# Kernel tuning notes

Hardware: AMD Instinct MI355X
Metric: run time of the kernel (lower is better)

The kernel has to match this reference:

```python
import jax, jax.numpy as jnp
import numpy as np

N_QUERY, N_BACKGND, DIM = 2048, 8192, 32


def setup_inputs() -> dict:
    key = jax.random.key(0)
    k0, k1, k2, k3 = jax.random.split(key, 4)
    x_backgnd = jax.random.normal(k0, (N_BACKGND, DIM), dtype=jnp.float32)
    y_backgnd = jax.random.normal(k1, (N_BACKGND,), dtype=jnp.float32)
    x_query = jax.random.normal(k2, (N_QUERY, DIM), dtype=jnp.float32)
    r = jax.random.uniform(k3, (N_QUERY, N_BACKGND), dtype=jnp.float32)
    sigma = jnp.array([0.1], dtype=jnp.float32)      # nn.Parameter init_sigma
    r_scale = jnp.array([3.0], dtype=jnp.float32)    # nn.Parameter init_r_scale
    w = jnp.ones((DIM,), dtype=jnp.float32)          # trainable weights matrix
    return {"x_backgnd": x_backgnd, "y_backgnd": y_backgnd, "x_query": x_query,
            "r": r, "sigma": sigma, "r_scale": r_scale, "w": w}


def reference(x_backgnd, y_backgnd, x_query, r, sigma, r_scale, w):
    # weighted Euclidean distance: ||(xq - xb) * w|| via the expansion trick,
    # avoiding the (n_query, n_backgnd, dim) difference tensor.
    xq = x_query * w           # (nq, d)
    xb = x_backgnd * w         # (nb, d)
    q2 = jnp.sum(xq * xq, axis=1, keepdims=True)        # (nq, 1)
    b2 = jnp.sum(xb * xb, axis=1)                        # (nb,)
    d2 = q2 + b2[None, :] - 2.0 * (xq @ xb.T)            # (nq, nb)
    dists = jnp.sqrt(jnp.maximum(d2, 0.0))
    # exp kernel with relationship bias, normalize, weighted sum
    k_vals = jnp.exp(-dists / sigma + r_scale * r)       # sigma, r_scale broadcast (1,)
    k_sum = jnp.sum(k_vals, axis=1, keepdims=True) + 1e-8
    weights = k_vals / k_sum
    y_pred = weights @ y_backgnd                          # (nq,)
    return y_pred
```

## Files before the change

kernel.cpp:

```cpp
#include <hip/hip_runtime.h>
#include <math.h>

#define NQ 2048
#define NB 8192
#define DIM 32

#define LOG2E 1.44269504088896340736f

typedef _Float16 half8 __attribute__((ext_vector_type(8)));
typedef float    f32x4 __attribute__((ext_vector_type(4)));

#define WS_ACC 0
#define WS_Q2  16384
#define WS_B2  24576
#define WS_XQH 57344
#define WS_XBH 188416

__global__ __launch_bounds__(256) void relnw_pre(
    const float* __restrict__ xq, const float* __restrict__ xb,
    const float* __restrict__ w,
    _Float16* __restrict__ XQh, _Float16* __restrict__ XBh,
    float* __restrict__ q2, float* __restrict__ b2)
{
    int i = blockIdx.x * 256 + threadIdx.x;
    const float* src; _Float16* dst; float* s2;
    if (i < NQ)            { src = xq + (size_t)i * DIM;        dst = XQh + (size_t)i * DIM;        s2 = q2 + i; }
    else if (i < NQ + NB)  { int j = i - NQ;
                             src = xb + (size_t)j * DIM;        dst = XBh + (size_t)j * DIM;        s2 = b2 + j; }
    else return;
    float s = 0.f;
#pragma unroll
    for (int d = 0; d < DIM; ++d) {
        float t = src[d] * w[d];
        _Float16 h = (_Float16)t;
        float th = (float)h;
        s = fmaf(th, th, s);
        dst[d] = h;
    }
    *s2 = s;
}

#define BT_PER_WAVE 16
#define BG_PER_WAVE (BT_PER_WAVE * 16)

__global__ __launch_bounds__(256) void relnw_main(
    const _Float16* __restrict__ XQh,
    const _Float16* __restrict__ XBh,
    const float* __restrict__ q2,
    const float* __restrict__ b2,
    const float* __restrict__ yb,
    const float* __restrict__ r,
    const float* __restrict__ sigma,
    const float* __restrict__ rscale,
    float* __restrict__ acc)
{
    const int tid  = threadIdx.x;
    const int lane = tid & 63;
    const int wid  = tid >> 6;
    const int m    = lane & 15;
    const int quad = lane >> 4;

    const int q0     = blockIdx.y * 16;
    const int bstart = (blockIdx.x * 4 + wid) * BG_PER_WAVE;

    const float c1 = -LOG2E / sigma[0];
    const float c2 =  LOG2E * rscale[0];

    const half8 afrag = *(const half8*)(XQh + (size_t)(q0 + m) * DIM + quad * 8);

    float q2r[4];
#pragma unroll
    for (int g = 0; g < 4; ++g) q2r[g] = q2[q0 + quad * 4 + g];

    const _Float16* xbp = XBh + (size_t)(bstart + m) * DIM + quad * 8;
    const float*    rp  = r + (size_t)(q0 + quad * 4) * NB + bstart + m;

    float sk[4]  = {0.f, 0.f, 0.f, 0.f};
    float sky[4] = {0.f, 0.f, 0.f, 0.f};

#pragma unroll
    for (int it = 0; it < BT_PER_WAVE; ++it) {
        const int bc = bstart + it * 16 + m;
        const half8 bfrag = *(const half8*)(xbp + (size_t)it * 16 * DIM);
        const float yv  = yb[bc];
        const float b2v = b2[bc];
        float rr[4];
#pragma unroll
        for (int g = 0; g < 4; ++g) rr[g] = rp[(size_t)g * NB + it * 16];

        f32x4 dot = __builtin_amdgcn_mfma_f32_16x16x32_f16(
            afrag, bfrag, (f32x4){0.f, 0.f, 0.f, 0.f}, 0, 0, 0);

#pragma unroll
        for (int g = 0; g < 4; ++g) {
            float d2 = fmaf(-2.f, dot[g], q2r[g] + b2v);
            d2 = fmaxf(d2, 0.f);
            float dist = __builtin_amdgcn_sqrtf(d2);
            float e = fmaf(dist, c1, rr[g] * c2);
            float k = __builtin_amdgcn_exp2f(e);
            sk[g] += k;
            sky[g] = fmaf(k, yv, sky[g]);
        }
    }

#pragma unroll
    for (int off = 1; off <= 8; off <<= 1) {
#pragma unroll
        for (int g = 0; g < 4; ++g) {
            sk[g]  += __shfl_xor(sk[g],  off, 64);
            sky[g] += __shfl_xor(sky[g], off, 64);
        }
    }
    if (m == 0) {
#pragma unroll
        for (int g = 0; g < 4; ++g) {
            atomicAdd(acc + (q0 + quad * 4 + g),      sk[g]);
            atomicAdd(acc + NQ + (q0 + quad * 4 + g), sky[g]);
        }
    }
}

__global__ __launch_bounds__(256) void relnw_finalize(
    const float* __restrict__ acc, float* __restrict__ out)
{
    int q = blockIdx.x * 256 + threadIdx.x;
    if (q < NQ)
        out[q] = acc[NQ + q] / (acc[q] + 1e-8f);
}

extern "C" void kernel_launch(void* const* d_in, const int* in_sizes, int n_in,
                              void* d_out, int out_size, void* d_ws, size_t ws_size,
                              hipStream_t stream) {
    const float* xb     = (const float*)d_in[0];
    const float* yb     = (const float*)d_in[1];
    const float* xq     = (const float*)d_in[2];
    const float* r      = (const float*)d_in[3];
    const float* sigma  = (const float*)d_in[4];
    const float* rscale = (const float*)d_in[5];
    const float* w      = (const float*)d_in[6];
    float* out = (float*)d_out;

    char* ws = (char*)d_ws;
    float*    acc = (float*)(ws + WS_ACC);
    float*    q2  = (float*)(ws + WS_Q2);
    float*    b2  = (float*)(ws + WS_B2);
    _Float16* XQh = (_Float16*)(ws + WS_XQH);
    _Float16* XBh = (_Float16*)(ws + WS_XBH);

    hipMemsetAsync(acc, 0, 2 * NQ * sizeof(float), stream);

    relnw_pre<<<(NQ + NB + 255) / 256, 256, 0, stream>>>(xq, xb, w, XQh, XBh, q2, b2);

    dim3 grid(NB / (4 * BG_PER_WAVE), NQ / 16);
    relnw_main<<<grid, 256, 0, stream>>>(XQh, XBh, q2, b2, yb, r, sigma, rscale, acc);

    relnw_finalize<<<(NQ + 255) / 256, 256, 0, stream>>>(acc, out);
}
```

Measured before the change: 117.0 us.

## Tile two query blocks per wave and fold accumulator zeroing into prep kernel

Each wave now computes two 16-query tiles against the same background fragment, so each loaded XB fragment, y and b2 value is reused across twice as many queries. The background span per wave is halved so the grid stays the same size. Separately, the accumulator memset is replaced by zeroing inside the preprocessing kernel, which drops one stream operation. Register pressure rises because accumulators and r loads are doubled, and the dominant r traffic is unchanged.

Measured after the change: 119.9 us. 2.4% more time.

```diff
diff --git a/kernel.cpp b/kernel.cpp
--- a/kernel.cpp
+++ b/kernel.cpp
@@ -20,13 +20,15 @@
     const float* __restrict__ xq, const float* __restrict__ xb,
     const float* __restrict__ w,
     _Float16* __restrict__ XQh, _Float16* __restrict__ XBh,
-    float* __restrict__ q2, float* __restrict__ b2)
+    float* __restrict__ q2, float* __restrict__ b2,
+    float* __restrict__ acc)
 {
     int i = blockIdx.x * 256 + threadIdx.x;
+    if (i < 2 * NQ) acc[i] = 0.f;
     const float* src; _Float16* dst; float* s2;
-    if (i < NQ)            { src = xq + (size_t)i * DIM;        dst = XQh + (size_t)i * DIM;        s2 = q2 + i; }
+    if (i < NQ)            { src = xq + (size_t)i * DIM;  dst = XQh + (size_t)i * DIM;  s2 = q2 + i; }
     else if (i < NQ + NB)  { int j = i - NQ;
-                             src = xb + (size_t)j * DIM;        dst = XBh + (size_t)j * DIM;        s2 = b2 + j; }
+                             src = xb + (size_t)j * DIM;  dst = XBh + (size_t)j * DIM;  s2 = b2 + j; }
     else return;
     float s = 0.f;
 #pragma unroll
@@ -40,8 +42,9 @@
     *s2 = s;
 }
 
-#define BT_PER_WAVE 16
+#define BT_PER_WAVE 8
 #define BG_PER_WAVE (BT_PER_WAVE * 16)
+#define QT 2
 
 __global__ __launch_bounds__(256) void relnw_main(
     const _Float16* __restrict__ XQh,
@@ -60,23 +63,26 @@
     const int m    = lane & 15;
     const int quad = lane >> 4;
 
-    const int q0     = blockIdx.y * 16;
+    const int q0     = blockIdx.y * (16 * QT);
     const int bstart = (blockIdx.x * 4 + wid) * BG_PER_WAVE;
 
     const float c1 = -LOG2E / sigma[0];
     const float c2 =  LOG2E * rscale[0];
 
-    const half8 afrag = *(const half8*)(XQh + (size_t)(q0 + m) * DIM + quad * 8);
-
-    float q2r[4];
+    half8 afrag[QT];
+    float q2r[QT][4];
 #pragma unroll
-    for (int g = 0; g < 4; ++g) q2r[g] = q2[q0 + quad * 4 + g];
+    for (int t = 0; t < QT; ++t) {
+        afrag[t] = *(const half8*)(XQh + (size_t)(q0 + t * 16 + m) * DIM + quad * 8);
+#pragma unroll
+        for (int g = 0; g < 4; ++g) q2r[t][g] = q2[q0 + t * 16 + quad * 4 + g];
+    }
 
     const _Float16* xbp = XBh + (size_t)(bstart + m) * DIM + quad * 8;
     const float*    rp  = r + (size_t)(q0 + quad * 4) * NB + bstart + m;
 
-    float sk[4]  = {0.f, 0.f, 0.f, 0.f};
-    float sky[4] = {0.f, 0.f, 0.f, 0.f};
+    float sk[QT][4]  = {};
+    float sky[QT][4] = {};
 
 #pragma unroll
     for (int it = 0; it < BT_PER_WAVE; ++it) {
@@ -84,39 +90,49 @@
         const half8 bfrag = *(const half8*)(xbp + (size_t)it * 16 * DIM);
         const float yv  = yb[bc];
         const float b2v = b2[bc];
-        float rr[4];
+        float rr[QT][4];
 #pragma unroll
-        for (int g = 0; g < 4; ++g) rr[g] = rp[(size_t)g * NB + it * 16];
-
-        f32x4 dot = __builtin_amdgcn_mfma_f32_16x16x32_f16(
-            afrag, bfrag, (f32x4){0.f, 0.f, 0.f, 0.f}, 0, 0, 0);
+        for (int t = 0; t < QT; ++t)
+#pragma unroll
+            for (int g = 0; g < 4; ++g)
+                rr[t][g] = rp[(size_t)(t * 16 + g) * NB + it * 16];
 
 #pragma unroll
-        for (int g = 0; g < 4; ++g) {
-            float d2 = fmaf(-2.f, dot[g], q2r[g] + b2v);
-            d2 = fmaxf(d2, 0.f);
-            float dist = __builtin_amdgcn_sqrtf(d2);
-            float e = fmaf(dist, c1, rr[g] * c2);
-            float k = __builtin_amdgcn_exp2f(e);
-            sk[g] += k;
-            sky[g] = fmaf(k, yv, sky[g]);
+        for (int t = 0; t < QT; ++t) {
+            f32x4 dot = __builtin_amdgcn_mfma_f32_16x16x32_f16(
+                afrag[t], bfrag, (f32x4){0.f, 0.f, 0.f, 0.f}, 0, 0, 0);
+#pragma unroll
+            for (int g = 0; g < 4; ++g) {
+                float d2 = fmaf(-2.f, dot[g], q2r[t][g] + b2v);
+                d2 = fmaxf(d2, 0.f);
+                float dist = __builtin_amdgcn_sqrtf(d2);
+                float e = fmaf(dist, c1, rr[t][g] * c2);
+                float k = __builtin_amdgcn_exp2f(e);
+                sk[t][g] += k;
+                sky[t][g] = fmaf(k, yv, sky[t][g]);
+            }
         }
     }
 
 #pragma unroll
     for (int off = 1; off <= 8; off <<= 1) {
 #pragma unroll
-        for (int g = 0; g < 4; ++g) {
-            sk[g]  += __shfl_xor(sk[g],  off, 64);
-            sky[g] += __shfl_xor(sky[g], off, 64);
-        }
+        for (int t = 0; t < QT; ++t)
+#pragma unroll
+            for (int g = 0; g < 4; ++g) {
+                sk[t][g]  += __shfl_xor(sk[t][g],  off, 64);
+                sky[t][g] += __shfl_xor(sky[t][g], off, 64);
+            }
     }
     if (m == 0) {
 #pragma unroll
-        for (int g = 0; g < 4; ++g) {
-            atomicAdd(acc + (q0 + quad * 4 + g),      sk[g]);
-            atomicAdd(acc + NQ + (q0 + quad * 4 + g), sky[g]);
-        }
+        for (int t = 0; t < QT; ++t)
+#pragma unroll
+            for (int g = 0; g < 4; ++g) {
+                int q = q0 + t * 16 + quad * 4 + g;
+                atomicAdd(acc + q,      sk[t][g]);
+                atomicAdd(acc + NQ + q, sky[t][g]);
+            }
     }
 }
 
@@ -147,11 +163,9 @@
     _Float16* XQh = (_Float16*)(ws + WS_XQH);
     _Float16* XBh = (_Float16*)(ws + WS_XBH);
 
-    hipMemsetAsync(acc, 0, 2 * NQ * sizeof(float), stream);
+    relnw_pre<<<(NQ + NB + 255) / 256, 256, 0, stream>>>(xq, xb, w, XQh, XBh, q2, b2, acc);
 
-    relnw_pre<<<(NQ + NB + 255) / 256, 256, 0, stream>>>(xq, xb, w, XQh, XBh, q2, b2);
-
-    dim3 grid(NB / (4 * BG_PER_WAVE), NQ / 16);
+    dim3 grid(NB / (4 * BG_PER_WAVE), NQ / (16 * QT));
     relnw_main<<<grid, 256, 0, stream>>>(XQh, XBh, q2, b2, yb, r, sigma, rscale, acc);
 
     relnw_finalize<<<(NQ + 255) / 256, 256, 0, stream>>>(acc, out);
```

## Fuse memset and finalize into pre/main kernels, fold distance terms into MFMA

Applied to the files above, without the earlier changes.

The accumulator zeroing moves into the preprocessing kernel, and the finalize kernel is replaced by a last-block-done counter inside the main kernel. This removes the memset and one kernel launch. The preprocessing kernel now uses four threads per row with vectorized float4 loads, half8 stores and a shuffle reduction. The background vectors are pre-scaled by -2 so the MFMA accumulator starts at q2+b2 and directly yields d2, saving per-element FMAs. The changes add an atomic counter, a threadfence and a serialized tail on the last block. Folding -2 into fp16 is exact.

Result: slower. 144.6 us (+23.5%).

```diff
diff --git a/kernel.cpp b/kernel.cpp
--- a/kernel.cpp
+++ b/kernel.cpp
@@ -11,37 +11,62 @@
 typedef float    f32x4 __attribute__((ext_vector_type(4)));
 
 #define WS_ACC 0
-#define WS_Q2  16384
-#define WS_B2  24576
-#define WS_XQH 57344
-#define WS_XBH 188416
+#define WS_CTR 16384
+#define WS_Q2  16448
+#define WS_B2  24640
+#define WS_XQH 57408
+#define WS_XBH 188480
 
 __global__ __launch_bounds__(256) void relnw_pre(
     const float* __restrict__ xq, const float* __restrict__ xb,
     const float* __restrict__ w,
     _Float16* __restrict__ XQh, _Float16* __restrict__ XBh,
-    float* __restrict__ q2, float* __restrict__ b2)
+    float* __restrict__ q2, float* __restrict__ b2,
+    float* __restrict__ acc, unsigned* __restrict__ ctr)
 {
-    int i = blockIdx.x * 256 + threadIdx.x;
-    const float* src; _Float16* dst; float* s2;
-    if (i < NQ)            { src = xq + (size_t)i * DIM;        dst = XQh + (size_t)i * DIM;        s2 = q2 + i; }
-    else if (i < NQ + NB)  { int j = i - NQ;
-                             src = xb + (size_t)j * DIM;        dst = XBh + (size_t)j * DIM;        s2 = b2 + j; }
-    else return;
+    const int tid = threadIdx.x;
+    const int gi  = blockIdx.x * 256 + tid;
+    if (gi < 2 * NQ) acc[gi] = 0.f;
+    if (gi == 0)     *ctr = 0u;
+
+    const int row = blockIdx.x * 64 + (tid >> 2);
+    const int p   = tid & 3;
+    if (row >= NQ + NB) return;
+
+    const float* src; _Float16* dst; float* s2; float scale;
+    if (row < NQ) { src = xq + (size_t)row * DIM;
+                    dst = XQh + (size_t)row * DIM; s2 = q2 + row; scale = 1.f; }
+    else          { int j = row - NQ;
+                    src = xb + (size_t)j * DIM;
+                    dst = XBh + (size_t)j * DIM;   s2 = b2 + j;   scale = -2.f; }
+
+    const float4 xa = ((const float4*)src)[p * 2];
+    const float4 xbv = ((const float4*)src)[p * 2 + 1];
+    const float4 wa = ((const float4*)w)[p * 2];
+    const float4 wb = ((const float4*)w)[p * 2 + 1];
+    const float xs[8] = {xa.x, xa.y, xa.z, xa.w, xbv.x, xbv.y, xbv.z, xbv.w};
+    const float ws_[8] = {wa.x, wa.y, wa.z, wa.w, wb.x, wb.y, wb.z, wb.w};
+
+    half8 h;
     float s = 0.f;
 #pragma unroll
-    for (int d = 0; d < DIM; ++d) {
-        float t = src[d] * w[d];
-        _Float16 h = (_Float16)t;
-        float th = (float)h;
+    for (int c = 0; c < 8; ++c) {
+        float t = xs[c] * ws_[c];
+        _Float16 hh = (_Float16)t;
+        float th = (float)hh;
         s = fmaf(th, th, s);
-        dst[d] = h;
+        h[c] = (_Float16)(th * scale);
     }
-    *s2 = s;
+    *(half8*)(dst + p * 8) = h;
+
+    s += __shfl_xor(s, 1, 64);
+    s += __shfl_xor(s, 2, 64);
+    if (p == 0) *s2 = s;
 }
 
 #define BT_PER_WAVE 16
 #define BG_PER_WAVE (BT_PER_WAVE * 16)
+#define NBLOCKS (8 * 128)
 
 __global__ __launch_bounds__(256) void relnw_main(
     const _Float16* __restrict__ XQh,
@@ -52,7 +77,9 @@
     const float* __restrict__ r,
     const float* __restrict__ sigma,
     const float* __restrict__ rscale,
-    float* __restrict__ acc)
+    float* __restrict__ acc,
+    unsigned* __restrict__ ctr,
+    float* __restrict__ out)
 {
     const int tid  = threadIdx.x;
     const int lane = tid & 63;
@@ -88,13 +115,16 @@
 #pragma unroll
         for (int g = 0; g < 4; ++g) rr[g] = rp[(size_t)g * NB + it * 16];
 
-        f32x4 dot = __builtin_amdgcn_mfma_f32_16x16x32_f16(
-            afrag, bfrag, (f32x4){0.f, 0.f, 0.f, 0.f}, 0, 0, 0);
+        f32x4 cin;
+#pragma unroll
+        for (int g = 0; g < 4; ++g) cin[g] = q2r[g] + b2v;
+
+        f32x4 d2v = __builtin_amdgcn_mfma_f32_16x16x32_f16(
+            afrag, bfrag, cin, 0, 0, 0);
 
 #pragma unroll
         for (int g = 0; g < 4; ++g) {
-            float d2 = fmaf(-2.f, dot[g], q2r[g] + b2v);
-            d2 = fmaxf(d2, 0.f);
+            float d2 = fmaxf(d2v[g], 0.f);
             float dist = __builtin_amdgcn_sqrtf(d2);
             float e = fmaf(dist, c1, rr[g] * c2);
             float k = __builtin_amdgcn_exp2f(e);
@@ -118,14 +148,21 @@
             atomicAdd(acc + NQ + (q0 + quad * 4 + g), sky[g]);
         }
     }
-}
 
-__global__ __launch_bounds__(256) void relnw_finalize(
-    const float* __restrict__ acc, float* __restrict__ out)
-{
-    int q = blockIdx.x * 256 + threadIdx.x;
-    if (q < NQ)
-        out[q] = acc[NQ + q] / (acc[q] + 1e-8f);
+    __syncthreads();
+    __shared__ int is_last;
+    if (tid == 0) {
+        __threadfence();
+        is_last = (atomicAdd(ctr, 1u) == NBLOCKS - 1);
+    }
+    __syncthreads();
+    if (is_last) {
+        for (int q = tid; q < NQ; q += 256) {
+            float skv  = atomicAdd(acc + q,      0.f);
+            float skyv = atomicAdd(acc + NQ + q, 0.f);
+            out[q] = skyv / (skv + 1e-8f);
+        }
+    }
 }
 
 extern "C" void kernel_launch(void* const* d_in, const int* in_sizes, int n_in,
@@ -142,17 +179,15 @@
 
     char* ws = (char*)d_ws;
     float*    acc = (float*)(ws + WS_ACC);
+    unsigned* ctr = (unsigned*)(ws + WS_CTR);
     float*    q2  = (float*)(ws + WS_Q2);
     float*    b2  = (float*)(ws + WS_B2);
     _Float16* XQh = (_Float16*)(ws + WS_XQH);
     _Float16* XBh = (_Float16*)(ws + WS_XBH);
 
-    hipMemsetAsync(acc, 0, 2 * NQ * sizeof(float), stream);
-
-    relnw_pre<<<(NQ + NB + 255) / 256, 256, 0, stream>>>(xq, xb, w, XQh, XBh, q2, b2);
+    relnw_pre<<<(NQ + NB) / 64, 256, 0, stream>>>(xq, xb, w, XQh, XBh, q2, b2, acc, ctr);
 
     dim3 grid(NB / (4 * BG_PER_WAVE), NQ / 16);
-    relnw_main<<<grid, 256, 0, stream>>>(XQh, XBh, q2, b2, yb, r, sigma, rscale, acc);
-
-    relnw_finalize<<<(NQ + 255) / 256, 256, 0, stream>>>(acc, out);
+    relnw_main<<<grid, 256, 0, stream>>>(XQh, XBh, q2, b2, yb, r, sigma, rscale,
+                                         acc, ctr, out);
 }
```
